# Kernel optimization log

Measured on AMD Instinct MI355X. Metric: run time of the kernel, lower is better.

## Reference

```python
import jax, jax.numpy as jnp
import numpy as np

DIM = 2048
HID = 1024
E = 16
TOP_K = 2
S_SHARED = 2


def setup_inputs() -> dict:
    key = jax.random.key(0)
    ks = jax.random.split(key, 6)
    scale = 0.02
    x = jax.random.normal(ks[0], (2, 2048, DIM), dtype=jnp.float32)
    gate_w = jax.random.normal(ks[1], (DIM, E), dtype=jnp.float32) * scale
    shared_w1 = jax.random.normal(ks[2], (S_SHARED, DIM, HID), dtype=jnp.float32) * scale
    shared_w2 = jax.random.normal(ks[3], (S_SHARED, HID, DIM), dtype=jnp.float32) * scale
    w1 = jax.random.normal(ks[4], (E, DIM, HID), dtype=jnp.float32) * scale
    w2 = jax.random.normal(ks[5], (E, HID, DIM), dtype=jnp.float32) * scale
    return {"x": x, "gate_w": gate_w, "shared_w1": shared_w1,
            "shared_w2": shared_w2, "w1": w1, "w2": w2}


def reference(x, gate_w, shared_w1, shared_w2, w1, w2):
    orig_shape = x.shape
    xf = x.reshape(-1, orig_shape[-1])  # [T, D]

    # Shared experts: sum of SiLU MLPs
    hs = jax.nn.silu(jnp.einsum('td,sdh->sth', xf, shared_w1))
    shared_out = jnp.einsum('sth,shd->td', hs, shared_w2)

    # Gating
    probs = jax.nn.softmax(xf @ gate_w, axis=-1)              # [T, E]
    weights, indices = jax.lax.top_k(probs, TOP_K)            # [T, K]
    weights = weights / weights.sum(axis=-1, keepdims=True)
    aux_loss = (probs.mean(axis=0) ** 2).sum() * E

    # Combine weights per (token, expert): top_k indices are distinct
    combine = (jax.nn.one_hot(indices, E, dtype=xf.dtype) *
               weights[..., None]).sum(axis=1)                # [T, E]

    # Dense all-expert compute (reference form of gather-GEMM-scatter)
    h = jax.nn.silu(jnp.einsum('td,edh->eth', xf, w1))        # [E, T, H]
    y = jnp.einsum('eth,ehd->etd', h, w2)                     # [E, T, D]
    routed_out = jnp.einsum('te,etd->td', combine, y)         # [T, D]

    out = (shared_out + routed_out).reshape(orig_shape)
    return out, aux_loss
```

## Files before the change

### kernel.cpp

```cpp
#include <hip/hip_runtime.h>
#include <math.h>

typedef unsigned short u16;
typedef __bf16 bf16x8 __attribute__((ext_vector_type(8)));
typedef float f32x4 __attribute__((ext_vector_type(4)));
typedef unsigned short u16x8 __attribute__((ext_vector_type(8)));

#define T_TOK 4096
#define DIMD 2048
#define HIDD 1024
#define NEXP 16
#define RMAX 10240
#define MAXBLK 96
#define BM 128
#define BN 256
#define BK 64

__device__ __forceinline__ u16 f2b(float f) {
  unsigned u = __builtin_bit_cast(unsigned, f);
  unsigned r = (u + 0x7FFFu + ((u >> 16) & 1u)) >> 16;
  return (u16)r;
}

__device__ __forceinline__ void gld16(const void* g, void* l) {
  __builtin_amdgcn_global_load_lds(
      (const __attribute__((address_space(1))) void*)g,
      (__attribute__((address_space(3))) void*)l, 16, 0, 0);
}


__global__ void k_pre(const float* __restrict__ x, u16* __restrict__ xb,
                      int* __restrict__ perm, int* __restrict__ cnt) {
  const int i = blockIdx.x * blockDim.x + threadIdx.x;
  const float4 v = ((const float4*)x)[i];
  union { u16 u[4]; unsigned long long q; } t;
  t.u[0] = f2b(v.x); t.u[1] = f2b(v.y); t.u[2] = f2b(v.z); t.u[3] = f2b(v.w);
  ((unsigned long long*)xb)[i] = t.q;
  if (i < RMAX) perm[i] = -1;
  if (i < NEXP) cnt[i] = 0;
}

__global__ __launch_bounds__(256)
void k_gate(const float* __restrict__ x, const float* __restrict__ gw,
            int* __restrict__ top2i, float* __restrict__ top2w,
            int* __restrict__ cnt, float* __restrict__ partial) {
  const int e = threadIdx.x & 15;
  const int tt = threadIdx.x >> 4;
  const int t = blockIdx.x * 16 + tt;
  const float* xp = x + (size_t)t * DIMD;
  float acc = 0.f;
#pragma unroll 8
  for (int k = 0; k < DIMD; ++k) acc = fmaf(xp[k], gw[k * NEXP + e], acc);
  __shared__ float lg[16][17];
  __shared__ float pr[16][17];
  lg[tt][e] = acc;
  __syncthreads();
  if (e == 0) {
    float l[16];
    float mx = -1e30f;
    for (int j = 0; j < 16; ++j) { l[j] = lg[tt][j]; mx = fmaxf(mx, l[j]); }
    float s = 0.f;
    for (int j = 0; j < 16; ++j) { l[j] = expf(l[j] - mx); s += l[j]; }
    const float inv = 1.f / s;
    float p1 = -1.f, p2 = -1.f; int i1 = 0, i2 = 0;
    for (int j = 0; j < 16; ++j) {
      const float p = l[j] * inv;
      pr[tt][j] = p;
      if (p > p1) { p2 = p1; i2 = i1; p1 = p; i1 = j; }
      else if (p > p2) { p2 = p; i2 = j; }
    }
    const float wsum = p1 + p2;
    top2i[t * 2 + 0] = i1;
    top2i[t * 2 + 1] = i2;
    top2w[t * 2 + 0] = p1 / wsum;
    top2w[t * 2 + 1] = p2 / wsum;
    atomicAdd(&cnt[i1], 1);
    atomicAdd(&cnt[i2], 1);
  }
  __syncthreads();
  if (tt == 0) {
    float s = 0.f;
    for (int j = 0; j < 16; ++j) s += pr[j][e];
    partial[blockIdx.x * 16 + e] = s;
  }
}

__global__ __launch_bounds__(256)
void k_sched(const int* __restrict__ cnt, const int* __restrict__ top2i,
             const float* __restrict__ top2w, const float* __restrict__ partial,
             int* __restrict__ tbl_e, int* __restrict__ tbl_r0,
             int* __restrict__ nblk, int* __restrict__ perm,
             float* __restrict__ wrow, int* __restrict__ slot2,
             float* __restrict__ auxOut) {
  __shared__ int offs[17];
  __shared__ int lfill[16];
  __shared__ float s[16][17];
  const int tid = threadIdx.x;
  if (tid == 0) {
    int o = 0, nb = 0;
    for (int e = 0; e < NEXP; ++e) {
      offs[e] = o;
      const int b = (cnt[e] + BM - 1) / BM;
      for (int i = 0; i < b; ++i) { tbl_e[nb] = e; tbl_r0[nb] = o + i * BM; ++nb; }
      o += b * BM;
    }
    offs[16] = o;
    nblk[0] = nb;
  }
  if (tid < 16) lfill[tid] = 0;
  __syncthreads();
  for (int id = tid; id < T_TOK * 2; id += 256) {
    const int e = top2i[id];
    const int pos = atomicAdd(&lfill[e], 1);
    const int r = offs[e] + pos;
    perm[r] = id >> 1;
    wrow[r] = top2w[id];
    slot2[id] = r;
  }
  const int e = tid & 15, c = tid >> 4;
  float a = 0.f;
  for (int b = c; b < 256; b += 16) a += partial[b * 16 + e];
  s[c][e] = a;
  __syncthreads();
  if (tid == 0) {
    float aux = 0.f;
    for (int j = 0; j < 16; ++j) {
      float tot = 0.f;
      for (int cc = 0; cc < 16; ++cc) tot += s[cc][j];
      const float m = tot / (float)T_TOK;
      aux += m * m;
    }
    auxOut[0] = aux * (float)NEXP;
  }
}

__global__ __launch_bounds__(256)
void k_trW(const float* __restrict__ w1, const float* __restrict__ w2,
           const float* __restrict__ sw1, const float* __restrict__ sw2,
           u16* __restrict__ w1t, u16* __restrict__ w2t,
           u16* __restrict__ sw1t, u16* __restrict__ sw2ct) {
  const int z = blockIdx.z;
  const float* W; u16* Wo; int K, N, ldo;
  if (z < 16) {
    W = w1 + (size_t)z * 2048 * 1024;
    Wo = w1t + (size_t)z * 1024 * 2048;
    K = 2048; N = 1024; ldo = 2048;
  } else if (z < 32) {
    W = w2 + (size_t)(z - 16) * 1024 * 2048;
    Wo = w2t + (size_t)(z - 16) * 2048 * 1024;
    K = 1024; N = 2048; ldo = 1024;
  } else if (z < 34) {
    W = sw1 + (size_t)(z - 32) * 2048 * 1024;
    Wo = sw1t + (size_t)(z - 32) * 1024 * 2048;
    K = 2048; N = 1024; ldo = 2048;
  } else {
    W = sw2 + (size_t)(z - 34) * 1024 * 2048;
    Wo = sw2ct + (size_t)(z - 34) * 1024;
    K = 1024; N = 2048; ldo = 2048;
  }
  const int n0 = blockIdx.x * 64, k0 = blockIdx.y * 64;
  if (n0 >= N || k0 >= K) return;
  __shared__ float t[64][65];
  {
    const int r = threadIdx.x >> 4;
    const int c = (threadIdx.x & 15) * 4;
#pragma unroll
    for (int p = 0; p < 4; ++p) {
      const int kk = p * 16 + r;
      const float4 v = *(const float4*)&W[(size_t)(k0 + kk) * N + n0 + c];
      t[kk][c] = v.x; t[kk][c + 1] = v.y; t[kk][c + 2] = v.z; t[kk][c + 3] = v.w;
    }
  }
  __syncthreads();
  {
    const int r2 = threadIdx.x >> 3;
    const int g8 = (threadIdx.x & 7) * 8;
#pragma unroll
    for (int p = 0; p < 2; ++p) {
      const int nn = p * 32 + r2;
      u16x8 o;
#pragma unroll
      for (int i = 0; i < 8; ++i) o[i] = f2b(t[g8 + i][nn]);
      *(u16x8*)&Wo[(size_t)(n0 + nn) * ldo + k0 + g8] = o;
    }
  }
}

__global__ __launch_bounds__(512)
void k_post(float* __restrict__ out, const float* __restrict__ rbLo,
            const float* __restrict__ rbHi, const int* __restrict__ slot2,
            const float* __restrict__ wrow) {
  const int t = blockIdx.x;
  const int d4 = threadIdx.x;
  const int s0 = slot2[t * 2], s1 = slot2[t * 2 + 1];
  const float w0 = wrow[s0], w1 = wrow[s1];
  const float4* r0 = (const float4*)(s0 < 8192 ? rbLo + (size_t)s0 * DIMD
                                               : rbHi + (size_t)(s0 - 8192) * DIMD);
  const float4* r1 = (const float4*)(s1 < 8192 ? rbLo + (size_t)s1 * DIMD
                                               : rbHi + (size_t)(s1 - 8192) * DIMD);
  float4* op = (float4*)(out + (size_t)t * DIMD);
  float4 o = op[d4];
  const float4 a = r0[d4], b = r1[d4];
  o.x += w0 * a.x + w1 * b.x;
  o.y += w0 * a.y + w1 * b.y;
  o.z += w0 * a.z + w1 * b.z;
  o.w += w0 * a.w + w1 * b.w;
  op[d4] = o;
}


__device__ __forceinline__ void stage_tile(
    const u16* gA0, const u16* gA1, const u16* gB0, const u16* gB1,
    const u16* gB2, const u16* gB3, int k0, u16* S, int b, int w) {
  u16* As = S + b * 24576;
  u16* Bs = As + 8192;
  gld16(gA0 + k0, As + w * 512);
  gld16(gA1 + k0, As + 4096 + w * 512);
  gld16(gB0 + k0, Bs + w * 512);
  gld16(gB1 + k0, Bs + 4096 + w * 512);
  gld16(gB2 + k0, Bs + 8192 + w * 512);
  gld16(gB3 + k0, Bs + 12288 + w * 512);
}

__device__ __forceinline__ void comp_tile(const u16* __restrict__ S, int b,
    const int (&aoff)[4][2], const int (&boff)[4][2], f32x4 (&acc)[4][4]) {
  const u16* As = S + b * 24576;
  const u16* Bs = As + 8192;
#pragma unroll
  for (int kh = 0; kh < 2; ++kh) {
    bf16x8 a[4], bq[4];
#pragma unroll
    for (int i = 0; i < 4; ++i) a[i] = *(const bf16x8*)(As + aoff[i][kh]);
#pragma unroll
    for (int j = 0; j < 4; ++j) bq[j] = *(const bf16x8*)(Bs + boff[j][kh]);
    __builtin_amdgcn_s_setprio(1);
#pragma unroll
    for (int i = 0; i < 4; ++i)
#pragma unroll
      for (int j = 0; j < 4; ++j)
        acc[i][j] = __builtin_amdgcn_mfma_f32_16x16x32_bf16(a[i], bq[j], acc[i][j], 0, 0, 0);
    __builtin_amdgcn_s_setprio(0);
  }
}

#define FENCE asm volatile("" ::: "memory")
#define VMW6  asm volatile("s_waitcnt vmcnt(6)" ::: "memory")
#define VMW0  asm volatile("s_waitcnt vmcnt(0)" ::: "memory")

__device__ __forceinline__ void gemm_pipe(
    const u16* gA0, const u16* gA1, const u16* gB0, const u16* gB1,
    const u16* gB2, const u16* gB3, int K, u16* S,
    const int (&aoff)[4][2], const int (&boff)[4][2],
    f32x4 (&acc)[4][4], int w) {
  const int nt = K >> 6;
  stage_tile(gA0, gA1, gB0, gB1, gB2, gB3, 0, S, 0, w);
  stage_tile(gA0, gA1, gB0, gB1, gB2, gB3, 64, S, 1, w);
  VMW6;
  __builtin_amdgcn_s_barrier();
  FENCE;
  for (int t = 0; t < nt - 2; ++t) {
    comp_tile(S, t & 1, aoff, boff, acc);
    FENCE;
    __builtin_amdgcn_s_barrier();
    FENCE;
    stage_tile(gA0, gA1, gB0, gB1, gB2, gB3, (t + 2) << 6, S, t & 1, w);
    VMW6;
    __builtin_amdgcn_s_barrier();
    FENCE;
  }
  comp_tile(S, 0, aoff, boff, acc);
  VMW0;
  __builtin_amdgcn_s_barrier();
  FENCE;
  comp_tile(S, 1, aoff, boff, acc);
}

__global__ __launch_bounds__(512, 2)
void k_up(const u16* __restrict__ xb, const u16* __restrict__ sw1t,
          const u16* __restrict__ w1t, u16* __restrict__ hbS,
          u16* __restrict__ hbR, const int* __restrict__ perm,
          const int* __restrict__ tbl_e, const int* __restrict__ tbl_r0,
          const int* __restrict__ nblk) {
  __shared__ u16 S[49152];
  const int bx = blockIdx.x, by = blockIdx.y;
  const int tid = threadIdx.x;
  const int w = tid >> 6, lane = tid & 63;
  const int lm = lane & 15, lq = lane >> 4;
  const int wm = w >> 2, wn = w & 3;
  const int srow = w * 8 + (lane >> 3);
  const int c8 = lane & 7;

  const bool routed = bx >= 32;
  int r0, ga0, ga1;
  const u16* Bb;
  if (!routed) {
    r0 = bx * BM;
    Bb = sw1t;
    ga0 = r0 + srow; ga1 = r0 + 64 + srow;
  } else {
    if (by >= 4) return;
    const int rbx = bx - 32;
    if (rbx >= *nblk) return;
    const int e = tbl_e[rbx];
    r0 = tbl_r0[rbx];
    Bb = w1t + (size_t)e * (size_t)HIDD * DIMD;
    const int p0 = perm[r0 + srow];      ga0 = (p0 < 0) ? 0 : p0;
    const int p1 = perm[r0 + 64 + srow]; ga1 = (p1 < 0) ? 0 : p1;
  }
  const int n0 = by * BN;
  const u16* gA0 = xb + (size_t)ga0 * DIMD + (c8 ^ ((srow >> 1) & 7)) * 8;
  const u16* gA1 = xb + (size_t)ga1 * DIMD + (c8 ^ (((64 + srow) >> 1) & 7)) * 8;
  const u16* gB[4];
#pragma unroll
  for (int p = 0; p < 4; ++p) {
    const int n = p * 64 + srow;
    gB[p] = Bb + (size_t)(n0 + n) * DIMD + (c8 ^ ((n >> 1) & 7)) * 8;
  }
  int aoff[4][2], boff[4][2];
#pragma unroll
  for (int i = 0; i < 4; ++i) {
    const int m = wm * 64 + i * 16 + lm;
    const int n = wn * 64 + i * 16 + lm;
#pragma unroll
    for (int kh = 0; kh < 2; ++kh) {
      aoff[i][kh] = m * 64 + (((kh << 2) | lq) ^ ((m >> 1) & 7)) * 8;
      boff[i][kh] = n * 64 + (((kh << 2) | lq) ^ ((n >> 1) & 7)) * 8;
    }
  }
  f32x4 acc[4][4];
#pragma unroll
  for (int i = 0; i < 4; ++i)
#pragma unroll
    for (int j = 0; j < 4; ++j) {
      acc[i][j][0] = 0.f; acc[i][j][1] = 0.f; acc[i][j][2] = 0.f; acc[i][j][3] = 0.f;
    }

  gemm_pipe(gA0, gA1, gB[0], gB[1], gB[2], gB[3], DIMD, S, aoff, boff, acc, w);

#pragma unroll
  for (int i = 0; i < 4; ++i) {
#pragma unroll
    for (int r = 0; r < 4; ++r) {
      const int row = r0 + wm * 64 + i * 16 + lq * 4 + r;
      u16* dst = routed ? &hbR[(size_t)row * HIDD] : &hbS[(size_t)row * DIMD];
#pragma unroll
      for (int j = 0; j < 4; ++j) {
        const int gc = n0 + wn * 64 + j * 16 + lm;
        const float v = acc[i][j][r];
        const float s = v / (1.f + expf(-v));
        dst[gc] = f2b(s);
      }
    }
  }
}

__global__ __launch_bounds__(512, 2)
void k_down(const u16* __restrict__ hbS, const u16* __restrict__ hbR,
            const u16* __restrict__ sw2ct, const u16* __restrict__ w2t,
            float* __restrict__ out, float* __restrict__ rbLo,
            float* __restrict__ rbHi, const int* __restrict__ tbl_e,
            const int* __restrict__ tbl_r0, const int* __restrict__ nblk) {
  __shared__ u16 S[49152];
  const int bx = blockIdx.x, by = blockIdx.y;
  const int tid = threadIdx.x;
  const int w = tid >> 6, lane = tid & 63;
  const int lm = lane & 15, lq = lane >> 4;
  const int wm = w >> 2, wn = w & 3;
  const int srow = w * 8 + (lane >> 3);
  const int c8 = lane & 7;

  const bool routed = bx >= 32;
  int r0, K, ld;
  const u16 *Ab, *Bb;
  if (!routed) {
    r0 = bx * BM;
    Ab = hbS; K = DIMD; ld = DIMD;
    Bb = sw2ct;
  } else {
    const int rbx = bx - 32;
    if (rbx >= *nblk) return;
    const int e = tbl_e[rbx];
    r0 = tbl_r0[rbx];
    Ab = hbR; K = HIDD; ld = HIDD;
    Bb = w2t + (size_t)e * (size_t)DIMD * HIDD;
  }
  const int n0 = by * BN;
  const u16* gA0 = Ab + (size_t)(r0 + srow) * ld + (c8 ^ ((srow >> 1) & 7)) * 8;
  const u16* gA1 = Ab + (size_t)(r0 + 64 + srow) * ld + (c8 ^ (((64 + srow) >> 1) & 7)) * 8;
  const u16* gB[4];
#pragma unroll
  for (int p = 0; p < 4; ++p) {
    const int n = p * 64 + srow;
    gB[p] = Bb + (size_t)(n0 + n) * ld + (c8 ^ ((n >> 1) & 7)) * 8;
  }
  int aoff[4][2], boff[4][2];
#pragma unroll
  for (int i = 0; i < 4; ++i) {
    const int m = wm * 64 + i * 16 + lm;
    const int n = wn * 64 + i * 16 + lm;
#pragma unroll
    for (int kh = 0; kh < 2; ++kh) {
      aoff[i][kh] = m * 64 + (((kh << 2) | lq) ^ ((m >> 1) & 7)) * 8;
      boff[i][kh] = n * 64 + (((kh << 2) | lq) ^ ((n >> 1) & 7)) * 8;
    }
  }
  f32x4 acc[4][4];
#pragma unroll
  for (int i = 0; i < 4; ++i)
#pragma unroll
    for (int j = 0; j < 4; ++j) {
      acc[i][j][0] = 0.f; acc[i][j][1] = 0.f; acc[i][j][2] = 0.f; acc[i][j][3] = 0.f;
    }

  gemm_pipe(gA0, gA1, gB[0], gB[1], gB[2], gB[3], K, S, aoff, boff, acc, w);

#pragma unroll
  for (int i = 0; i < 4; ++i) {
#pragma unroll
    for (int r = 0; r < 4; ++r) {
      const int rr = r0 + wm * 64 + i * 16 + lq * 4 + r;
      float* dst;
      if (!routed) dst = out + (size_t)rr * DIMD;
      else dst = (rr < 8192) ? rbLo + (size_t)rr * DIMD
                             : rbHi + (size_t)(rr - 8192) * DIMD;
#pragma unroll
      for (int j = 0; j < 4; ++j) {
        const int gc = n0 + wn * 64 + j * 16 + lm;
        dst[gc] = acc[i][j][r];
      }
    }
  }
}


extern "C" void kernel_launch(void* const* d_in, const int* in_sizes, int n_in,
                              void* d_out, int out_size, void* d_ws, size_t ws_size,
                              hipStream_t stream) {
  const float* x   = (const float*)d_in[0];
  const float* gw  = (const float*)d_in[1];
  const float* sw1 = (const float*)d_in[2];
  const float* sw2 = (const float*)d_in[3];
  const float* w1  = (const float*)d_in[4];
  const float* w2  = (const float*)d_in[5];
  float* out = (float*)d_out;

  char* ws = (char*)d_ws;
  u16* xb    = (u16*)(ws);
  u16* hbS   = (u16*)(ws + (size_t)( 16 << 20));
  u16* hbR   = (u16*)(ws + (size_t)( 32 << 20));
  u16* sw1t  = (u16*)(ws + (size_t)( 56 << 20));
  u16* sw2ct = (u16*)(ws + (size_t)( 64 << 20));
  u16* w1t   = (u16*)(ws + (size_t)( 72 << 20));
  u16* w2t   = (u16*)(ws + (size_t)(136 << 20));
  float* rbLo = (float*)(ws + (size_t)( 72 << 20));
  float* rbHi = (float*)(ws);
  char* p = ws + (size_t)(200 << 20);
  int*   top2i   = (int*)p;    p += T_TOK * 2 * 4;
  float* top2w   = (float*)p;  p += T_TOK * 2 * 4;
  int*   perm    = (int*)p;    p += RMAX * 4;
  float* wrow    = (float*)p;  p += RMAX * 4;
  int*   slot2   = (int*)p;    p += T_TOK * 2 * 4;
  int*   cnt     = (int*)p;    p += 16 * 4;
  int*   tbl_e   = (int*)p;    p += MAXBLK * 4;
  int*   tbl_r0  = (int*)p;    p += MAXBLK * 4;
  int*   nblk    = (int*)p;    p += 16 * 4;
  float* partial = (float*)p;  p += 256 * 16 * 4;

  k_pre<<<(T_TOK * DIMD / 4) / 256, 256, 0, stream>>>(x, xb, perm, cnt);
  k_gate<<<T_TOK / 16, 256, 0, stream>>>(x, gw, top2i, top2w, cnt, partial);
  k_sched<<<1, 256, 0, stream>>>(cnt, top2i, top2w, partial, tbl_e, tbl_r0,
                                 nblk, perm, wrow, slot2,
                                 out + (size_t)T_TOK * DIMD);
  k_trW<<<dim3(32, 32, 36), 256, 0, stream>>>(w1, w2, sw1, sw2,
                                              w1t, w2t, sw1t, sw2ct);
  k_up<<<dim3(32 + MAXBLK, 8), 512, 0, stream>>>(xb, sw1t, w1t, hbS, hbR,
                                                 perm, tbl_e, tbl_r0, nblk);
  k_down<<<dim3(32 + MAXBLK, 8), 512, 0, stream>>>(hbS, hbR, sw2ct, w2t, out,
                                                   rbLo, rbHi, tbl_e, tbl_r0, nblk);
  k_post<<<T_TOK, 512, 0, stream>>>(out, rbLo, rbHi, slot2, wrow);
}
```

Before: 762.7 us.

## Shrink GEMM tiles to 128x128x32 with 256-thread blocks and token-ordered scatter

Reworks the up and down GEMM kernels from 128x256x64 tiles with 512 threads to 128x128x32 tiles with 256 threads. This cuts LDS use per block, allows four blocks per CU and doubles the grid in the N dimension, at the cost of less data reuse per tile and more barriers per K step. The routed down-projection now scatters rows directly into a token-ordered buffer through a new perm2 map, so k_post reads two contiguous rows per token instead of going through slot and weight indirection. The weight-transpose kernel's z ordering is also changed so w2 and the shared weights are converted first.

After: 800.1 us. 4.9% more time.

```diff
diff --git a/kernel.cpp b/kernel.cpp
--- a/kernel.cpp
+++ b/kernel.cpp
@@ -13,8 +13,8 @@
 #define RMAX 10240
 #define MAXBLK 96
 #define BM 128
-#define BN 256
-#define BK 64
+#define BN 128
+#define BK 32
 
 __device__ __forceinline__ u16 f2b(float f) {
   unsigned u = __builtin_bit_cast(unsigned, f);
@@ -30,13 +30,14 @@
 
 
 __global__ void k_pre(const float* __restrict__ x, u16* __restrict__ xb,
-                      int* __restrict__ perm, int* __restrict__ cnt) {
+                      int* __restrict__ perm, int* __restrict__ perm2,
+                      int* __restrict__ cnt) {
   const int i = blockIdx.x * blockDim.x + threadIdx.x;
   const float4 v = ((const float4*)x)[i];
   union { u16 u[4]; unsigned long long q; } t;
   t.u[0] = f2b(v.x); t.u[1] = f2b(v.y); t.u[2] = f2b(v.z); t.u[3] = f2b(v.w);
   ((unsigned long long*)xb)[i] = t.q;
-  if (i < RMAX) perm[i] = -1;
+  if (i < RMAX) { perm[i] = -1; perm2[i] = -1; }
   if (i < NEXP) cnt[i] = 0;
 }
 
@@ -90,8 +91,7 @@
              const float* __restrict__ top2w, const float* __restrict__ partial,
              int* __restrict__ tbl_e, int* __restrict__ tbl_r0,
              int* __restrict__ nblk, int* __restrict__ perm,
-             float* __restrict__ wrow, int* __restrict__ slot2,
-             float* __restrict__ auxOut) {
+             int* __restrict__ perm2, float* __restrict__ auxOut) {
   __shared__ int offs[17];
   __shared__ int lfill[16];
   __shared__ float s[16][17];
@@ -114,8 +114,7 @@
     const int pos = atomicAdd(&lfill[e], 1);
     const int r = offs[e] + pos;
     perm[r] = id >> 1;
-    wrow[r] = top2w[id];
-    slot2[id] = r;
+    perm2[r] = id;
   }
   const int e = tid & 15, c = tid >> 4;
   float a = 0.f;
@@ -142,21 +141,17 @@
   const int z = blockIdx.z;
   const float* W; u16* Wo; int K, N, ldo;
   if (z < 16) {
-    W = w1 + (size_t)z * 2048 * 1024;
-    Wo = w1t + (size_t)z * 1024 * 2048;
+    W = w2 + (size_t)z * 1024 * 2048;  Wo = w2t + (size_t)z * 2048 * 1024;
+    K = 1024; N = 2048; ldo = 1024;
+  } else if (z < 18) {
+    W = sw1 + (size_t)(z - 16) * 2048 * 1024;  Wo = sw1t + (size_t)(z - 16) * 1024 * 2048;
     K = 2048; N = 1024; ldo = 2048;
-  } else if (z < 32) {
-    W = w2 + (size_t)(z - 16) * 1024 * 2048;
-    Wo = w2t + (size_t)(z - 16) * 2048 * 1024;
-    K = 1024; N = 2048; ldo = 1024;
-  } else if (z < 34) {
-    W = sw1 + (size_t)(z - 32) * 2048 * 1024;
-    Wo = sw1t + (size_t)(z - 32) * 1024 * 2048;
+  } else if (z < 20) {
+    W = sw2 + (size_t)(z - 18) * 1024 * 2048;  Wo = sw2ct + (size_t)(z - 18) * 1024;
+    K = 1024; N = 2048; ldo = 2048;
+  } else {
+    W = w1 + (size_t)(z - 20) * 2048 * 1024;  Wo = w1t + (size_t)(z - 20) * 1024 * 2048;
     K = 2048; N = 1024; ldo = 2048;
-  } else {
-    W = sw2 + (size_t)(z - 34) * 1024 * 2048;
-    Wo = sw2ct + (size_t)(z - 34) * 1024;
-    K = 1024; N = 2048; ldo = 2048;
   }
   const int n0 = blockIdx.x * 64, k0 = blockIdx.y * 64;
   if (n0 >= N || k0 >= K) return;
@@ -187,20 +182,15 @@
 }
 
 __global__ __launch_bounds__(512)
-void k_post(float* __restrict__ out, const float* __restrict__ rbLo,
-            const float* __restrict__ rbHi, const int* __restrict__ slot2,
-            const float* __restrict__ wrow) {
+void k_post(float* __restrict__ out, const float* __restrict__ rb,
+            const float* __restrict__ top2w) {
   const int t = blockIdx.x;
   const int d4 = threadIdx.x;
-  const int s0 = slot2[t * 2], s1 = slot2[t * 2 + 1];
-  const float w0 = wrow[s0], w1 = wrow[s1];
-  const float4* r0 = (const float4*)(s0 < 8192 ? rbLo + (size_t)s0 * DIMD
-                                               : rbHi + (size_t)(s0 - 8192) * DIMD);
-  const float4* r1 = (const float4*)(s1 < 8192 ? rbLo + (size_t)s1 * DIMD
-                                               : rbHi + (size_t)(s1 - 8192) * DIMD);
+  const float w0 = top2w[t * 2], w1 = top2w[t * 2 + 1];
+  const float4 a = ((const float4*)(rb + (size_t)(2 * t) * DIMD))[d4];
+  const float4 b = ((const float4*)(rb + (size_t)(2 * t + 1) * DIMD))[d4];
   float4* op = (float4*)(out + (size_t)t * DIMD);
   float4 o = op[d4];
-  const float4 a = r0[d4], b = r1[d4];
   o.x += w0 * a.x + w1 * b.x;
   o.y += w0 * a.y + w1 * b.y;
   o.z += w0 * a.z + w1 * b.z;
@@ -209,123 +199,110 @@
 }
 
 
-__device__ __forceinline__ void stage_tile(
-    const u16* gA0, const u16* gA1, const u16* gB0, const u16* gB1,
-    const u16* gB2, const u16* gB3, int k0, u16* S, int b, int w) {
-  u16* As = S + b * 24576;
-  u16* Bs = As + 8192;
-  gld16(gA0 + k0, As + w * 512);
-  gld16(gA1 + k0, As + 4096 + w * 512);
-  gld16(gB0 + k0, Bs + w * 512);
-  gld16(gB1 + k0, Bs + 4096 + w * 512);
-  gld16(gB2 + k0, Bs + 8192 + w * 512);
-  gld16(gB3 + k0, Bs + 12288 + w * 512);
-}
-
-__device__ __forceinline__ void comp_tile(const u16* __restrict__ S, int b,
-    const int (&aoff)[4][2], const int (&boff)[4][2], f32x4 (&acc)[4][4]) {
-  const u16* As = S + b * 24576;
-  const u16* Bs = As + 8192;
-#pragma unroll
-  for (int kh = 0; kh < 2; ++kh) {
-    bf16x8 a[4], bq[4];
-#pragma unroll
-    for (int i = 0; i < 4; ++i) a[i] = *(const bf16x8*)(As + aoff[i][kh]);
-#pragma unroll
-    for (int j = 0; j < 4; ++j) bq[j] = *(const bf16x8*)(Bs + boff[j][kh]);
-    __builtin_amdgcn_s_setprio(1);
-#pragma unroll
-    for (int i = 0; i < 4; ++i)
-#pragma unroll
-      for (int j = 0; j < 4; ++j)
-        acc[i][j] = __builtin_amdgcn_mfma_f32_16x16x32_bf16(a[i], bq[j], acc[i][j], 0, 0, 0);
-    __builtin_amdgcn_s_setprio(0);
-  }
-}
-
 #define FENCE asm volatile("" ::: "memory")
-#define VMW6  asm volatile("s_waitcnt vmcnt(6)" ::: "memory")
+#define VMW4  asm volatile("s_waitcnt vmcnt(4)" ::: "memory")
 #define VMW0  asm volatile("s_waitcnt vmcnt(0)" ::: "memory")
-
-__device__ __forceinline__ void gemm_pipe(
-    const u16* gA0, const u16* gA1, const u16* gB0, const u16* gB1,
-    const u16* gB2, const u16* gB3, int K, u16* S,
-    const int (&aoff)[4][2], const int (&boff)[4][2],
-    f32x4 (&acc)[4][4], int w) {
-  const int nt = K >> 6;
-  stage_tile(gA0, gA1, gB0, gB1, gB2, gB3, 0, S, 0, w);
-  stage_tile(gA0, gA1, gB0, gB1, gB2, gB3, 64, S, 1, w);
-  VMW6;
-  __builtin_amdgcn_s_barrier();
-  FENCE;
+#define BARR  do { FENCE; __builtin_amdgcn_s_barrier(); FENCE; } while (0)
+
+struct SP { const u16* a[2]; const u16* b[2]; };
+
+__device__ __forceinline__ void stage_t(const SP& sp, u16* S, int buf,
+                                        int w, int k) {
+  u16* As = S + buf * 8192;
+  u16* Bs = As + 4096;
+#pragma unroll
+  for (int j = 0; j < 2; ++j) {
+    gld16(sp.a[j] + k, As + (w * 2 + j) * 512);
+    gld16(sp.b[j] + k, Bs + (w * 2 + j) * 512);
+  }
+}
+
+__device__ __forceinline__ void comp_t(const u16* __restrict__ S, int buf,
+    const int (&aoff)[4], const int (&boff)[4], f32x4 (&acc)[4][4]) {
+  const u16* As = S + buf * 8192;
+  bf16x8 af[4], bq[4];
+#pragma unroll
+  for (int i = 0; i < 4; ++i) af[i] = *(const bf16x8*)(As + aoff[i]);
+#pragma unroll
+  for (int j = 0; j < 4; ++j) bq[j] = *(const bf16x8*)(As + 4096 + boff[j]);
+  __builtin_amdgcn_s_setprio(1);
+#pragma unroll
+  for (int i = 0; i < 4; ++i)
+#pragma unroll
+    for (int j = 0; j < 4; ++j)
+      acc[i][j] = __builtin_amdgcn_mfma_f32_16x16x32_bf16(af[i], bq[j], acc[i][j], 0, 0, 0);
+  __builtin_amdgcn_s_setprio(0);
+}
+
+__device__ __forceinline__ void gemm_r2(const SP& sp, int K, u16* S,
+    const int (&aoff)[4], const int (&boff)[4], f32x4 (&acc)[4][4], int w) {
+  const int nt = K >> 5;
+  stage_t(sp, S, 0, w, 0);
+  stage_t(sp, S, 1, w, BK);
+  VMW4;
+  BARR;
+  int cur = 0;
   for (int t = 0; t < nt - 2; ++t) {
-    comp_tile(S, t & 1, aoff, boff, acc);
-    FENCE;
-    __builtin_amdgcn_s_barrier();
-    FENCE;
-    stage_tile(gA0, gA1, gB0, gB1, gB2, gB3, (t + 2) << 6, S, t & 1, w);
-    VMW6;
-    __builtin_amdgcn_s_barrier();
-    FENCE;
-  }
-  comp_tile(S, 0, aoff, boff, acc);
+    comp_t(S, cur, aoff, boff, acc);
+    BARR;
+    stage_t(sp, S, cur, w, (t + 2) << 5);
+    VMW4;
+    BARR;
+    cur ^= 1;
+  }
+  comp_t(S, cur, aoff, boff, acc);
   VMW0;
-  __builtin_amdgcn_s_barrier();
-  FENCE;
-  comp_tile(S, 1, aoff, boff, acc);
-}
-
-__global__ __launch_bounds__(512, 2)
+  BARR;
+  comp_t(S, cur ^ 1, aoff, boff, acc);
+}
+
+
+__global__ __launch_bounds__(256, 4)
 void k_up(const u16* __restrict__ xb, const u16* __restrict__ sw1t,
           const u16* __restrict__ w1t, u16* __restrict__ hbS,
           u16* __restrict__ hbR, const int* __restrict__ perm,
           const int* __restrict__ tbl_e, const int* __restrict__ tbl_r0,
           const int* __restrict__ nblk) {
-  __shared__ u16 S[49152];
+  __shared__ u16 S[16384];
   const int bx = blockIdx.x, by = blockIdx.y;
   const int tid = threadIdx.x;
   const int w = tid >> 6, lane = tid & 63;
   const int lm = lane & 15, lq = lane >> 4;
-  const int wm = w >> 2, wn = w & 3;
-  const int srow = w * 8 + (lane >> 3);
-  const int c8 = lane & 7;
+  const int wm = w >> 1, wn = w & 1;
 
   const bool routed = bx >= 32;
-  int r0, ga0, ga1;
-  const u16* Bb;
+  int r0; const u16* Bb;
   if (!routed) {
     r0 = bx * BM;
     Bb = sw1t;
-    ga0 = r0 + srow; ga1 = r0 + 64 + srow;
   } else {
-    if (by >= 4) return;
+    if (by >= 8) return;
     const int rbx = bx - 32;
     if (rbx >= *nblk) return;
     const int e = tbl_e[rbx];
     r0 = tbl_r0[rbx];
     Bb = w1t + (size_t)e * (size_t)HIDD * DIMD;
-    const int p0 = perm[r0 + srow];      ga0 = (p0 < 0) ? 0 : p0;
-    const int p1 = perm[r0 + 64 + srow]; ga1 = (p1 < 0) ? 0 : p1;
   }
   const int n0 = by * BN;
-  const u16* gA0 = xb + (size_t)ga0 * DIMD + (c8 ^ ((srow >> 1) & 7)) * 8;
-  const u16* gA1 = xb + (size_t)ga1 * DIMD + (c8 ^ (((64 + srow) >> 1) & 7)) * 8;
-  const u16* gB[4];
-#pragma unroll
-  for (int p = 0; p < 4; ++p) {
-    const int n = p * 64 + srow;
-    gB[p] = Bb + (size_t)(n0 + n) * DIMD + (c8 ^ ((n >> 1) & 7)) * 8;
-  }
-  int aoff[4][2], boff[4][2];
+
+  SP sp;
+#pragma unroll
+  for (int j = 0; j < 2; ++j) {
+    const int lrow = (w * 2 + j) * 16 + (lane >> 2);
+    const int co = ((lane & 3) ^ ((lrow >> 1) & 3)) * 8;
+    int ga;
+    if (!routed) ga = r0 + lrow;
+    else { const int p = perm[r0 + lrow]; ga = (p < 0) ? 0 : p; }
+    sp.a[j] = xb + (size_t)ga * DIMD + co;
+    sp.b[j] = Bb + (size_t)(n0 + lrow) * DIMD + co;
+  }
+  int aoff[4], boff[4];
 #pragma unroll
   for (int i = 0; i < 4; ++i) {
-    const int m = wm * 64 + i * 16 + lm;
-    const int n = wn * 64 + i * 16 + lm;
-#pragma unroll
-    for (int kh = 0; kh < 2; ++kh) {
-      aoff[i][kh] = m * 64 + (((kh << 2) | lq) ^ ((m >> 1) & 7)) * 8;
-      boff[i][kh] = n * 64 + (((kh << 2) | lq) ^ ((n >> 1) & 7)) * 8;
-    }
+    const int ra = wm * 64 + i * 16 + lm;
+    const int rb_ = wn * 64 + i * 16 + lm;
+    aoff[i] = ra * 32 + ((lq ^ ((ra >> 1) & 3)) * 8);
+    boff[i] = rb_ * 32 + ((lq ^ ((rb_ >> 1) & 3)) * 8);
   }
   f32x4 acc[4][4];
 #pragma unroll
@@ -335,14 +312,14 @@
       acc[i][j][0] = 0.f; acc[i][j][1] = 0.f; acc[i][j][2] = 0.f; acc[i][j][3] = 0.f;
     }
 
-  gemm_pipe(gA0, gA1, gB[0], gB[1], gB[2], gB[3], DIMD, S, aoff, boff, acc, w);
+  gemm_r2(sp, DIMD, S, aoff, boff, acc, w);
 
 #pragma unroll
   for (int i = 0; i < 4; ++i) {
 #pragma unroll
     for (int r = 0; r < 4; ++r) {
       const int row = r0 + wm * 64 + i * 16 + lq * 4 + r;
-      u16* dst = routed ? &hbR[(size_t)row * HIDD] : &hbS[(size_t)row * DIMD];
+      u16* dst = routed ? hbR + (size_t)row * HIDD : hbS + (size_t)row * DIMD;
 #pragma unroll
       for (int j = 0; j < 4; ++j) {
         const int gc = n0 + wn * 64 + j * 16 + lm;
@@ -354,20 +331,18 @@
   }
 }
 
-__global__ __launch_bounds__(512, 2)
+__global__ __launch_bounds__(256, 4)
 void k_down(const u16* __restrict__ hbS, const u16* __restrict__ hbR,
             const u16* __restrict__ sw2ct, const u16* __restrict__ w2t,
-            float* __restrict__ out, float* __restrict__ rbLo,
-            float* __restrict__ rbHi, const int* __restrict__ tbl_e,
+            float* __restrict__ out, float* __restrict__ rb,
+            const int* __restrict__ perm2, const int* __restrict__ tbl_e,
             const int* __restrict__ tbl_r0, const int* __restrict__ nblk) {
-  __shared__ u16 S[49152];
+  __shared__ u16 S[16384];
   const int bx = blockIdx.x, by = blockIdx.y;
   const int tid = threadIdx.x;
   const int w = tid >> 6, lane = tid & 63;
   const int lm = lane & 15, lq = lane >> 4;
-  const int wm = w >> 2, wn = w & 3;
-  const int srow = w * 8 + (lane >> 3);
-  const int c8 = lane & 7;
+  const int wm = w >> 1, wn = w & 1;
 
   const bool routed = bx >= 32;
   int r0, K, ld;
@@ -385,24 +360,22 @@
     Bb = w2t + (size_t)e * (size_t)DIMD * HIDD;
   }
   const int n0 = by * BN;
-  const u16* gA0 = Ab + (size_t)(r0 + srow) * ld + (c8 ^ ((srow >> 1) & 7)) * 8;
-  const u16* gA1 = Ab + (size_t)(r0 + 64 + srow) * ld + (c8 ^ (((64 + srow) >> 1) & 7)) * 8;
-  const u16* gB[4];
-#pragma unroll
-  for (int p = 0; p < 4; ++p) {
-    const int n = p * 64 + srow;
-    gB[p] = Bb + (size_t)(n0 + n) * ld + (c8 ^ ((n >> 1) & 7)) * 8;
-  }
-  int aoff[4][2], boff[4][2];
+
+  SP sp;
+#pragma unroll
+  for (int j = 0; j < 2; ++j) {
+    const int lrow = (w * 2 + j) * 16 + (lane >> 2);
+    const int co = ((lane & 3) ^ ((lrow >> 1) & 3)) * 8;
+    sp.a[j] = Ab + (size_t)(r0 + lrow) * ld + co;
+    sp.b[j] = Bb + (size_t)(n0 + lrow) * ld + co;
+  }
+  int aoff[4], boff[4];
 #pragma unroll
   for (int i = 0; i < 4; ++i) {
-    const int m = wm * 64 + i * 16 + lm;
-    const int n = wn * 64 + i * 16 + lm;
-#pragma unroll
-    for (int kh = 0; kh < 2; ++kh) {
-      aoff[i][kh] = m * 64 + (((kh << 2) | lq) ^ ((m >> 1) & 7)) * 8;
-      boff[i][kh] = n * 64 + (((kh << 2) | lq) ^ ((n >> 1) & 7)) * 8;
-    }
+    const int ra = wm * 64 + i * 16 + lm;
+    const int rb_ = wn * 64 + i * 16 + lm;
+    aoff[i] = ra * 32 + ((lq ^ ((ra >> 1) & 3)) * 8);
+    boff[i] = rb_ * 32 + ((lq ^ ((rb_ >> 1) & 3)) * 8);
   }
   f32x4 acc[4][4];
 #pragma unroll
@@ -412,21 +385,26 @@
       acc[i][j][0] = 0.f; acc[i][j][1] = 0.f; acc[i][j][2] = 0.f; acc[i][j][3] = 0.f;
     }
 
-  gemm_pipe(gA0, gA1, gB[0], gB[1], gB[2], gB[3], K, S, aoff, boff, acc, w);
+  gemm_r2(sp, K, S, aoff, boff, acc, w);
 
 #pragma unroll
   for (int i = 0; i < 4; ++i) {
 #pragma unroll
     for (int r = 0; r < 4; ++r) {
-      const int rr = r0 + wm * 64 + i * 16 + lq * 4 + r;
-      float* dst;
-      if (!routed) dst = out + (size_t)rr * DIMD;
-      else dst = (rr < 8192) ? rbLo + (size_t)rr * DIMD
-                             : rbHi + (size_t)(rr - 8192) * DIMD;
-#pragma unroll
-      for (int j = 0; j < 4; ++j) {
-        const int gc = n0 + wn * 64 + j * 16 + lm;
-        dst[gc] = acc[i][j][r];
+      const int row = r0 + wm * 64 + i * 16 + lq * 4 + r;
+      if (!routed) {
+        float* dst = out + (size_t)row * DIMD;
+#pragma unroll
+        for (int j = 0; j < 4; ++j)
+          dst[n0 + wn * 64 + j * 16 + lm] = acc[i][j][r];
+      } else {
+        const int id2 = perm2[row];
+        if (id2 >= 0) {
+          float* dst = rb + (size_t)id2 * DIMD;
+#pragma unroll
+          for (int j = 0; j < 4; ++j)
+            dst[n0 + wn * 64 + j * 16 + lm] = acc[i][j][r];
+        }
       }
     }
   }
@@ -452,30 +430,27 @@
   u16* sw2ct = (u16*)(ws + (size_t)( 64 << 20));
   u16* w1t   = (u16*)(ws + (size_t)( 72 << 20));
   u16* w2t   = (u16*)(ws + (size_t)(136 << 20));
-  float* rbLo = (float*)(ws + (size_t)( 72 << 20));
-  float* rbHi = (float*)(ws);
+  float* rb  = (float*)(ws + (size_t)( 72 << 20));
   char* p = ws + (size_t)(200 << 20);
   int*   top2i   = (int*)p;    p += T_TOK * 2 * 4;
   float* top2w   = (float*)p;  p += T_TOK * 2 * 4;
   int*   perm    = (int*)p;    p += RMAX * 4;
-  float* wrow    = (float*)p;  p += RMAX * 4;
-  int*   slot2   = (int*)p;    p += T_TOK * 2 * 4;
+  int*   perm2   = (int*)p;    p += RMAX * 4;
   int*   cnt     = (int*)p;    p += 16 * 4;
   int*   tbl_e   = (int*)p;    p += MAXBLK * 4;
   int*   tbl_r0  = (int*)p;    p += MAXBLK * 4;
   int*   nblk    = (int*)p;    p += 16 * 4;
   float* partial = (float*)p;  p += 256 * 16 * 4;
 
-  k_pre<<<(T_TOK * DIMD / 4) / 256, 256, 0, stream>>>(x, xb, perm, cnt);
+  k_pre<<<(T_TOK * DIMD / 4) / 256, 256, 0, stream>>>(x, xb, perm, perm2, cnt);
   k_gate<<<T_TOK / 16, 256, 0, stream>>>(x, gw, top2i, top2w, cnt, partial);
   k_sched<<<1, 256, 0, stream>>>(cnt, top2i, top2w, partial, tbl_e, tbl_r0,
-                                 nblk, perm, wrow, slot2,
-                                 out + (size_t)T_TOK * DIMD);
+                                 nblk, perm, perm2, out + (size_t)T_TOK * DIMD);
   k_trW<<<dim3(32, 32, 36), 256, 0, stream>>>(w1, w2, sw1, sw2,
                                               w1t, w2t, sw1t, sw2ct);
-  k_up<<<dim3(32 + MAXBLK, 8), 512, 0, stream>>>(xb, sw1t, w1t, hbS, hbR,
-                                                 perm, tbl_e, tbl_r0, nblk);
-  k_down<<<dim3(32 + MAXBLK, 8), 512, 0, stream>>>(hbS, hbR, sw2ct, w2t, out,
-                                                   rbLo, rbHi, tbl_e, tbl_r0, nblk);
-  k_post<<<T_TOK, 512, 0, stream>>>(out, rbLo, rbHi, slot2, wrow);
-}
+  k_up<<<dim3(32 + MAXBLK, 16), 256, 0, stream>>>(xb, sw1t, w1t, hbS, hbR,
+                                                  perm, tbl_e, tbl_r0, nblk);
+  k_down<<<dim3(32 + MAXBLK, 16), 256, 0, stream>>>(hbS, hbR, sw2ct, w2t, out,
+                                                    rb, perm2, tbl_e, tbl_r0, nblk);
+  k_post<<<T_TOK, 512, 0, stream>>>(out, rb, top2w);
+}
```
